# Optimization experiments

Measured on AMD Instinct MI355X. Metric: run time of the kernel, lower is better.

The kernel has to match this reference:

```python
import jax, jax.numpy as jnp
import numpy as np
from jax import lax

IN_CH = 256
FILTERS_PER_CH = 2            # expansion = 1 -> 2 filters per input channel
INTER_CH = IN_CH * FILTERS_PER_CH
BUTTERFLY_SIZE = 8
BUTTERFLIES = INTER_CH // 2 // BUTTERFLY_SIZE  # 32
WING = BUTTERFLY_SIZE // 2                      # 4


def setup_inputs() -> dict:
    key = jax.random.key(0)
    k1, k2 = jax.random.split(key)
    x = jax.random.normal(k1, (32, IN_CH, 56, 56), dtype=jnp.float32)
    # depthwise conv weight, PyTorch OIHW with groups=IN_CH: (INTER_CH, 1, 3, 3)
    w = jax.random.normal(k2, (INTER_CH, 1, 3, 3), dtype=jnp.float32) * 0.1
    return {"x": x, "w": w}


def reference(x, w):
    # grouped (depthwise, channel multiplier 2) conv, stride 1, pad 1, no bias
    y = lax.conv_general_dilated(
        x, w,
        window_strides=(1, 1),
        padding=[(1, 1), (1, 1)],
        feature_group_count=IN_CH,
        dimension_numbers=("NCHW", "OIHW", "NCHW"),
    )  # (B, INTER_CH, H, W); channels group-major: 2i,2i+1 from input i
    B, C2, H, W = y.shape
    # extract_sequences: consecutive channels alternate between the two outputs
    y = y.reshape(B, C2 // 2, 2, H, W)
    x1 = y[:, :, 0]  # (B, IN_CH, H, W)
    x2 = y[:, :, 1]
    # swap_wings: within each butterfly, swap the two wings
    s = x2.reshape(B, BUTTERFLIES, 2, WING, H, W)
    x2 = jnp.flip(s, axis=2).reshape(B, C2 // 2, H, W)
    return x1 + x2
```

## Files before the change

### kernel.cpp

```cpp
#include <hip/hip_runtime.h>

#define IN_CH 256
#define IMG_W 56
#define BAND  28
#define LROWS 29
#define CH_F  (LROWS * IMG_W)

typedef __attribute__((address_space(1))) const void GBuf;
typedef __attribute__((address_space(3))) void LBuf;

__global__ __launch_bounds__(256, 6) void dwconv_butterfly(
    const float* __restrict__ x, const float* __restrict__ wgt,
    float* __restrict__ out)
{
    __shared__ float lds[2 * CH_F];

    const int tid  = threadIdx.x;
    const int p    = blockIdx.x;
    const int b    = blockIdx.y;
    const int band = blockIdx.z;
    const int c0   = ((p >> 2) << 3) | (p & 3);
    const int c1   = c0 ^ 4;

    const size_t chan = 56u * 56u;
    const float* x0 = x + ((size_t)b * IN_CH + c0) * chan;
    const float* x1 = x + ((size_t)b * IN_CH + c1) * chan;
    float* o0 = out + ((size_t)b * IN_CH + c0) * chan + (size_t)band * BAND * IMG_W;
    float* o1 = out + ((size_t)b * IN_CH + c1) * chan + (size_t)band * BAND * IMG_W;

    const int gbase = band ? 27 : 0;
    const float* g0 = x0 + gbase * IMG_W;
    const float* g1 = x1 + gbase * IMG_W;

    {
        const int wbase = tid & ~63;
#pragma unroll
        for (int k = 0; k < 3; ++k) {
            const int q = tid + 256 * k;
            const float* src = (q < 406) ? (g0 + 4 * q) : (g1 + 4 * (q - 406));
            __builtin_amdgcn_global_load_lds((GBuf*)src,
                (LBuf*)&lds[4 * (256 * k + wbase)], 16, 0, 0);
        }
        if (tid < 44) {
            const float* src = g1 + 4 * (768 + tid - 406);
            __builtin_amdgcn_global_load_lds((GBuf*)src,
                (LBuf*)&lds[4 * 768], 16, 0, 0);
        }
    }

    float wa[9], wb[9], wc[9], wd[9];
    {
        const float* pa = wgt + (size_t)(2 * c0) * 9;
        const float* pb = wgt + (size_t)(2 * c1 + 1) * 9;
        const float* pc = wgt + (size_t)(2 * c1) * 9;
        const float* pd = wgt + (size_t)(2 * c0 + 1) * 9;
#pragma unroll
        for (int i = 0; i < 9; ++i) {
            wa[i] = pa[i]; wb[i] = pb[i]; wc[i] = pc[i]; wd[i] = pd[i];
        }
    }

    __syncthreads();

    if (tid < 196) {
        const int rp  = tid / 14;
        const int w0  = (tid - rp * 14) * 4;
        const int oh0 = rp * 2;
        const int rbase = oh0 - 1 + band;

        const bool has_l = (w0 > 0);
        const bool has_r = (w0 < 52);
        const int  col_l = has_l ? (w0 - 1) : 0;
        const int  col_r = has_r ? (w0 + 4) : 55;

        float W[4][12];
#pragma unroll
        for (int rr = 0; rr < 4; ++rr) {
            const int r  = rbase + rr;
            const bool zr = (rr == 0) ? (r < 0) : ((rr == 3) ? (r > 28) : false);
            const int  rc = (rr == 0) ? (r < 0 ? 0 : r) : ((rr == 3) ? (r > 28 ? 28 : r) : r);
            const float* p0 = &lds[rc * IMG_W + w0];
            const float* p1 = p0 + CH_F;
            const float4 a0 = *(const float4*)p0;
            const float4 a1 = *(const float4*)p1;
            const float l0 = lds[rc * IMG_W + col_l];
            const float r0 = lds[rc * IMG_W + col_r];
            const float l1 = lds[CH_F + rc * IMG_W + col_l];
            const float r1 = lds[CH_F + rc * IMG_W + col_r];
            W[rr][0]  = (zr || !has_l) ? 0.f : l0;
            W[rr][1]  = zr ? 0.f : a0.x;
            W[rr][2]  = zr ? 0.f : a0.y;
            W[rr][3]  = zr ? 0.f : a0.z;
            W[rr][4]  = zr ? 0.f : a0.w;
            W[rr][5]  = (zr || !has_r) ? 0.f : r0;
            W[rr][6]  = (zr || !has_l) ? 0.f : l1;
            W[rr][7]  = zr ? 0.f : a1.x;
            W[rr][8]  = zr ? 0.f : a1.y;
            W[rr][9]  = zr ? 0.f : a1.z;
            W[rr][10] = zr ? 0.f : a1.w;
            W[rr][11] = (zr || !has_r) ? 0.f : r1;
        }

        float acc[2][8];
#pragma unroll
        for (int j = 0; j < 2; ++j)
#pragma unroll
            for (int i = 0; i < 8; ++i) acc[j][i] = 0.f;

#pragma unroll
        for (int j = 0; j < 2; ++j) {
#pragma unroll
            for (int kh = 0; kh < 3; ++kh) {
                const int rw = j + kh;
#pragma unroll
                for (int kw = 0; kw < 3; ++kw) {
                    const float fa = wa[kh * 3 + kw], fb = wb[kh * 3 + kw];
                    const float fc = wc[kh * 3 + kw], fd = wd[kh * 3 + kw];
#pragma unroll
                    for (int i = 0; i < 4; ++i) {
                        const float u0 = W[rw][i + kw];
                        const float u1 = W[rw][6 + i + kw];
                        acc[j][i]     += u0 * fa + u1 * fb;
                        acc[j][4 + i] += u1 * fc + u0 * fd;
                    }
                }
            }
        }

#pragma unroll
        for (int j = 0; j < 2; ++j) {
            float* q0 = o0 + (oh0 + j) * IMG_W + w0;
            float* q1 = o1 + (oh0 + j) * IMG_W + w0;
            *(float4*)q0 = make_float4(acc[j][0], acc[j][1], acc[j][2], acc[j][3]);
            *(float4*)q1 = make_float4(acc[j][4], acc[j][5], acc[j][6], acc[j][7]);
        }
    }
}

extern "C" void kernel_launch(void* const* d_in, const int* in_sizes, int n_in,
                              void* d_out, int out_size, void* d_ws, size_t ws_size,
                              hipStream_t stream) {
    const float* x = (const float*)d_in[0];
    const float* w = (const float*)d_in[1];
    float* out = (float*)d_out;

    dim3 grid(IN_CH / 2, 32, 2);
    dim3 block(256);
    dwconv_butterfly<<<grid, block, 0, stream>>>(x, w, out);
}
```

Measured before the change: 186.8 us.

## Drop LDS staging and read halo rows directly from global per full image

```diff
diff --git a/kernel.cpp b/kernel.cpp
--- a/kernel.cpp
+++ b/kernel.cpp
@@ -2,138 +2,105 @@
 
 #define IN_CH 256
 #define IMG_W 56
-#define BAND  28
-#define LROWS 29
-#define CH_F  (LROWS * IMG_W)
+typedef float f4 __attribute__((ext_vector_type(4)));
 
-typedef __attribute__((address_space(1))) const void GBuf;
-typedef __attribute__((address_space(3))) void LBuf;
-
-__global__ __launch_bounds__(256, 6) void dwconv_butterfly(
+__global__ __launch_bounds__(448, 5) void dwconv_butterfly(
     const float* __restrict__ x, const float* __restrict__ wgt,
     float* __restrict__ out)
 {
-    __shared__ float lds[2 * CH_F];
+    const int tid = threadIdx.x;
+    const int pb  = blockIdx.x;
+    const int p   = pb & 127;
+    const int b   = pb >> 7;
+    const int c0  = ((p >> 2) << 3) | (p & 3);
+    const int c1  = c0 ^ 4;
 
-    const int tid  = threadIdx.x;
-    const int p    = blockIdx.x;
-    const int b    = blockIdx.y;
-    const int band = blockIdx.z;
-    const int c0   = ((p >> 2) << 3) | (p & 3);
-    const int c1   = c0 ^ 4;
-
-    const size_t chan = 56u * 56u;
+    const size_t chan = (size_t)IMG_W * IMG_W;
     const float* x0 = x + ((size_t)b * IN_CH + c0) * chan;
     const float* x1 = x + ((size_t)b * IN_CH + c1) * chan;
-    float* o0 = out + ((size_t)b * IN_CH + c0) * chan + (size_t)band * BAND * IMG_W;
-    float* o1 = out + ((size_t)b * IN_CH + c1) * chan + (size_t)band * BAND * IMG_W;
+    float* o0 = out + ((size_t)b * IN_CH + c0) * chan;
+    float* o1 = out + ((size_t)b * IN_CH + c1) * chan;
 
-    const int gbase = band ? 27 : 0;
-    const float* g0 = x0 + gbase * IMG_W;
-    const float* g1 = x1 + gbase * IMG_W;
+    const float* pwa = wgt + (size_t)(2 * c0) * 9;
+    const float* pwb = wgt + (size_t)(2 * c1 + 1) * 9;
+    const float* pwc = wgt + (size_t)(2 * c1) * 9;
+    const float* pwd = wgt + (size_t)(2 * c0 + 1) * 9;
+    float wa[9], wb[9], wc[9], wd[9];
+#pragma unroll
+    for (int i = 0; i < 9; ++i) {
+        wa[i] = pwa[i]; wb[i] = pwb[i]; wc[i] = pwc[i]; wd[i] = pwd[i];
+    }
 
-    {
-        const int wbase = tid & ~63;
+    if (tid >= 392) return;
+    const int s  = tid % 14;
+    const int rp = tid / 14;
+    const int w0 = 4 * s;
+    const bool has_l = (s > 0), has_r = (s < 13);
+    const int  col_l = has_l ? w0 - 1 : 0;
+    const int  col_r = has_r ? w0 + 4 : IMG_W - 1;
+
+    f4    va[4], vb[4];
+    float la[4], ra[4], lb[4], rb[4];
+    bool  rv[4];
 #pragma unroll
-        for (int k = 0; k < 3; ++k) {
-            const int q = tid + 256 * k;
-            const float* src = (q < 406) ? (g0 + 4 * q) : (g1 + 4 * (q - 406));
-            __builtin_amdgcn_global_load_lds((GBuf*)src,
-                (LBuf*)&lds[4 * (256 * k + wbase)], 16, 0, 0);
-        }
-        if (tid < 44) {
-            const float* src = g1 + 4 * (768 + tid - 406);
-            __builtin_amdgcn_global_load_lds((GBuf*)src,
-                (LBuf*)&lds[4 * 768], 16, 0, 0);
+    for (int k = 0; k < 4; ++k) {
+        const int ir  = 2 * rp - 1 + k;
+        rv[k] = (unsigned)ir < 56u;
+        const int irc = ir < 0 ? 0 : (ir > 55 ? 55 : ir);
+        const float* r0 = x0 + irc * IMG_W;
+        const float* r1 = x1 + irc * IMG_W;
+        va[k] = *(const f4*)(r0 + w0);
+        vb[k] = *(const f4*)(r1 + w0);
+        la[k] = r0[col_l];
+        ra[k] = r0[col_r];
+        lb[k] = r1[col_l];
+        rb[k] = r1[col_r];
+    }
+
+    float acc[2][8];
+#pragma unroll
+    for (int j = 0; j < 2; ++j)
+#pragma unroll
+        for (int i = 0; i < 8; ++i) acc[j][i] = 0.f;
+
+#pragma unroll
+    for (int k = 0; k < 4; ++k) {
+        const bool z = !rv[k];
+        float W0[6], W1[6];
+        W0[0] = (z || !has_l) ? 0.f : la[k];
+        W0[1] = z ? 0.f : va[k].x;  W0[2] = z ? 0.f : va[k].y;
+        W0[3] = z ? 0.f : va[k].z;  W0[4] = z ? 0.f : va[k].w;
+        W0[5] = (z || !has_r) ? 0.f : ra[k];
+        W1[0] = (z || !has_l) ? 0.f : lb[k];
+        W1[1] = z ? 0.f : vb[k].x;  W1[2] = z ? 0.f : vb[k].y;
+        W1[3] = z ? 0.f : vb[k].z;  W1[4] = z ? 0.f : vb[k].w;
+        W1[5] = (z || !has_r) ? 0.f : rb[k];
+#pragma unroll
+        for (int j = 0; j < 2; ++j) {
+            const int kh = k - j;
+            if (kh < 0 || kh > 2) continue;
+#pragma unroll
+            for (int kw = 0; kw < 3; ++kw) {
+                const float fa = wa[kh * 3 + kw], fb = wb[kh * 3 + kw];
+                const float fc = wc[kh * 3 + kw], fd = wd[kh * 3 + kw];
+#pragma unroll
+                for (int i = 0; i < 4; ++i) {
+                    const float u0 = W0[i + kw];
+                    const float u1 = W1[i + kw];
+                    acc[j][i]     += u0 * fa + u1 * fb;
+                    acc[j][4 + i] += u1 * fc + u0 * fd;
+                }
+            }
         }
     }
 
-    float wa[9], wb[9], wc[9], wd[9];
-    {
-        const float* pa = wgt + (size_t)(2 * c0) * 9;
-        const float* pb = wgt + (size_t)(2 * c1 + 1) * 9;
-        const float* pc = wgt + (size_t)(2 * c1) * 9;
-        const float* pd = wgt + (size_t)(2 * c0 + 1) * 9;
 #pragma unroll
-        for (int i = 0; i < 9; ++i) {
-            wa[i] = pa[i]; wb[i] = pb[i]; wc[i] = pc[i]; wd[i] = pd[i];
-        }
-    }
-
-    __syncthreads();
-
-    if (tid < 196) {
-        const int rp  = tid / 14;
-        const int w0  = (tid - rp * 14) * 4;
-        const int oh0 = rp * 2;
-        const int rbase = oh0 - 1 + band;
-
-        const bool has_l = (w0 > 0);
-        const bool has_r = (w0 < 52);
-        const int  col_l = has_l ? (w0 - 1) : 0;
-        const int  col_r = has_r ? (w0 + 4) : 55;
-
-        float W[4][12];
-#pragma unroll
-        for (int rr = 0; rr < 4; ++rr) {
-            const int r  = rbase + rr;
-            const bool zr = (rr == 0) ? (r < 0) : ((rr == 3) ? (r > 28) : false);
-            const int  rc = (rr == 0) ? (r < 0 ? 0 : r) : ((rr == 3) ? (r > 28 ? 28 : r) : r);
-            const float* p0 = &lds[rc * IMG_W + w0];
-            const float* p1 = p0 + CH_F;
-            const float4 a0 = *(const float4*)p0;
-            const float4 a1 = *(const float4*)p1;
-            const float l0 = lds[rc * IMG_W + col_l];
-            const float r0 = lds[rc * IMG_W + col_r];
-            const float l1 = lds[CH_F + rc * IMG_W + col_l];
-            const float r1 = lds[CH_F + rc * IMG_W + col_r];
-            W[rr][0]  = (zr || !has_l) ? 0.f : l0;
-            W[rr][1]  = zr ? 0.f : a0.x;
-            W[rr][2]  = zr ? 0.f : a0.y;
-            W[rr][3]  = zr ? 0.f : a0.z;
-            W[rr][4]  = zr ? 0.f : a0.w;
-            W[rr][5]  = (zr || !has_r) ? 0.f : r0;
-            W[rr][6]  = (zr || !has_l) ? 0.f : l1;
-            W[rr][7]  = zr ? 0.f : a1.x;
-            W[rr][8]  = zr ? 0.f : a1.y;
-            W[rr][9]  = zr ? 0.f : a1.z;
-            W[rr][10] = zr ? 0.f : a1.w;
-            W[rr][11] = (zr || !has_r) ? 0.f : r1;
-        }
-
-        float acc[2][8];
-#pragma unroll
-        for (int j = 0; j < 2; ++j)
-#pragma unroll
-            for (int i = 0; i < 8; ++i) acc[j][i] = 0.f;
-
-#pragma unroll
-        for (int j = 0; j < 2; ++j) {
-#pragma unroll
-            for (int kh = 0; kh < 3; ++kh) {
-                const int rw = j + kh;
-#pragma unroll
-                for (int kw = 0; kw < 3; ++kw) {
-                    const float fa = wa[kh * 3 + kw], fb = wb[kh * 3 + kw];
-                    const float fc = wc[kh * 3 + kw], fd = wd[kh * 3 + kw];
-#pragma unroll
-                    for (int i = 0; i < 4; ++i) {
-                        const float u0 = W[rw][i + kw];
-                        const float u1 = W[rw][6 + i + kw];
-                        acc[j][i]     += u0 * fa + u1 * fb;
-                        acc[j][4 + i] += u1 * fc + u0 * fd;
-                    }
-                }
-            }
-        }
-
-#pragma unroll
-        for (int j = 0; j < 2; ++j) {
-            float* q0 = o0 + (oh0 + j) * IMG_W + w0;
-            float* q1 = o1 + (oh0 + j) * IMG_W + w0;
-            *(float4*)q0 = make_float4(acc[j][0], acc[j][1], acc[j][2], acc[j][3]);
-            *(float4*)q1 = make_float4(acc[j][4], acc[j][5], acc[j][6], acc[j][7]);
-        }
+    for (int j = 0; j < 2; ++j) {
+        const int orow = 2 * rp + j;
+        f4 v0; v0.x = acc[j][0]; v0.y = acc[j][1]; v0.z = acc[j][2]; v0.w = acc[j][3];
+        f4 v1; v1.x = acc[j][4]; v1.y = acc[j][5]; v1.z = acc[j][6]; v1.w = acc[j][7];
+        *(f4*)(o0 + orow * IMG_W + w0) = v0;
+        *(f4*)(o1 + orow * IMG_W + w0) = v1;
     }
 }
 
@@ -144,7 +111,7 @@
     const float* w = (const float*)d_in[1];
     float* out = (float*)d_out;
 
-    dim3 grid(IN_CH / 2, 32, 2);
-    dim3 block(256);
+    dim3 grid(128 * 32);
+    dim3 block(448);
     dwconv_butterfly<<<grid, block, 0, stream>>>(x, w, out);
 }
```

Result: slower. 195.2 us (+4.5%).
